# Kernel optimization log

Hardware: AMD Instinct MI355X
Metric: run time of the kernel (lower is better)

## Reference

```python
import jax, jax.numpy as jnp
import numpy as np

N_NODES = 10000
N_EDGES = 160000
HIDDEN = 64
NUM_RBF = 32
Q_DIM = 8
CUTOFF_UPPER = 5.0


def silu(x):
    return x * jax.nn.sigmoid(x)


def tensor_norm(X):
    # X: [n, 3, 3, H] -> [n, H] (Frobenius norm squared over the 3x3 dims)
    return (X * X).sum(axis=(1, 2))


def decompose_tensor(X):
    # X: [n, 3, 3, H] -> I: [n, H] (trace/3), A: antisym [n,3,3,H], S: sym traceless [n,3,3,H]
    eye = jnp.eye(3, dtype=X.dtype)[None, :, :, None]
    I = jnp.einsum('naah->nh', X) / 3.0
    Xt = X.transpose(0, 2, 1, 3)
    A = 0.5 * (X - Xt)
    S = 0.5 * (X + Xt) - I[:, None, None, :] * eye
    return I, A, S


def compose_tensor(I, A, S):
    eye = jnp.eye(3, dtype=A.dtype)[None, :, :, None]
    return I[:, None, None, :] * eye + A + S


def tmm(P, Q):
    # 3x3 matmul per (atom, channel): [n,3,3,H] x [n,3,3,H] -> [n,3,3,H]
    return jnp.einsum('nach,ncbh->nabh', P, Q)


def setup_inputs() -> dict:
    key = jax.random.key(0)
    ks = jax.random.split(key, 16)
    H = HIDDEN
    inp = {
        'X': jax.random.normal(ks[0], (N_NODES, 3, 3, H), jnp.float32),
        'charges': jax.random.normal(ks[1], (N_NODES, Q_DIM), jnp.float32),
        'edge_weight': jax.random.uniform(ks[2], (N_EDGES,), jnp.float32) * CUTOFF_UPPER,
        'edge_attr': jax.random.normal(ks[3], (N_EDGES, NUM_RBF), jnp.float32),
        'edge_index': jax.random.randint(ks[4], (2, N_EDGES), 0, N_NODES, jnp.int32),
    }
    d_in = NUM_RBF + 2 * Q_DIM
    inp['Ws1'] = jax.random.normal(ks[5], (d_in, H), jnp.float32) / np.sqrt(d_in).astype(np.float32)
    inp['bs1'] = jnp.zeros((H,), jnp.float32)
    inp['Ws2'] = jax.random.normal(ks[6], (H, 2 * H), jnp.float32) / np.sqrt(H).astype(np.float32)
    inp['bs2'] = jnp.zeros((2 * H,), jnp.float32)
    inp['Ws3'] = jax.random.normal(ks[7], (2 * H, 3 * H), jnp.float32) / np.sqrt(2 * H).astype(np.float32)
    inp['bs3'] = jnp.zeros((3 * H,), jnp.float32)
    for i in range(6):
        inp['Wt%d' % i] = jax.random.normal(ks[8 + i], (H, H), jnp.float32) / np.sqrt(H).astype(np.float32)
    return inp


def reference(X, charges, edge_weight, edge_attr, Ws1, bs1, Ws2, bs2, Ws3, bs3,
              Wt0, Wt1, Wt2, Wt3, Wt4, Wt5, edge_index):
    H = HIDDEN
    n = X.shape[0]
    row, col = edge_index[0], edge_index[1]
    # cosine cutoff (cutoff_lower = 0)
    C = 0.5 * (jnp.cos(edge_weight * (jnp.pi / CUTOFF_UPPER)) + 1.0)
    C = C * (edge_weight < CUTOFF_UPPER).astype(X.dtype)
    # edge scalar MLP on [rbf, q_i, q_j]
    h = jnp.concatenate([edge_attr, charges[row], charges[col]], axis=-1)
    h = silu(h @ Ws1 + bs1)
    h = silu(h @ Ws2 + bs2)
    h = silu(h @ Ws3 + bs3)
    w = (h * C[:, None]).reshape(h.shape[0], 3, H)  # [E, 3, H]
    # normalize node tensors
    X = X / (tensor_norm(X) + 1.0)[:, None, None, :]
    I, A, S = decompose_tensor(X)
    I = I @ Wt0
    A = A @ Wt1
    S = S @ Wt2
    Y = compose_tensor(I, A, S)
    # message passing: gather I/A/S at source (edge_index[1]), weight per component, scatter-add at dest (edge_index[0])
    eye = jnp.eye(3, dtype=X.dtype)[None, :, :, None]
    msg_e = ((w[:, 0] * I[col])[:, None, None, :] * eye
             + w[:, 1][:, None, None, :] * A[col]
             + w[:, 2][:, None, None, :] * S[col])  # [E, 3, 3, H]
    msg = jax.ops.segment_sum(msg_e, row, num_segments=n)  # [n, 3, 3, H]
    # O(3): C = msg @ Y + Y @ msg (3x3 matmul per channel)
    Cm = tmm(msg, Y) + tmm(Y, msg)
    I2, A2, S2 = decompose_tensor(Cm)
    normp1 = tensor_norm(Cm) + 1.0
    I2 = I2 / normp1
    A2 = A2 / normp1[:, None, None, :]
    S2 = S2 / normp1[:, None, None, :]
    I2 = I2 @ Wt3
    A2 = A2 @ Wt4
    S2 = S2 @ Wt5
    dX = compose_tensor(I2, A2, S2)
    return X + dX + tmm(dX, dX)
```

## Files before the change

kernel.cpp:

```cpp
#include <hip/hip_runtime.h>
#include <math.h>

#define HD 64

typedef _Float16 half8 __attribute__((ext_vector_type(8)));
typedef _Float16 half4v __attribute__((ext_vector_type(4)));
typedef float floatx4 __attribute__((ext_vector_type(4)));

__device__ __forceinline__ float silu_f(float x) {
    return x * __builtin_amdgcn_rcpf(1.0f + __expf(-x));
}

__global__ __launch_bounds__(256) void pre_wconv(
    const float* __restrict__ X,
    const float* __restrict__ Wt0, const float* __restrict__ Wt1, const float* __restrict__ Wt2,
    float* __restrict__ Tn, _Float16* __restrict__ TnH, int N, int nbPre,
    const float* __restrict__ Ws1, const float* __restrict__ Ws2, const float* __restrict__ Ws3,
    _Float16* __restrict__ W1f, _Float16* __restrict__ W2f, _Float16* __restrict__ W3f)
{
    if (blockIdx.x >= nbPre) {
        int id = (blockIdx.x - nbPre) * 256 + threadIdx.x;
        if (id < 4096) {
            int i = id & 7, l = (id >> 3) & 63, t = id >> 9;
            int s = t >> 2, nt = t & 3;
            int k = s * 32 + (l >> 4) * 8 + i;
            int n = nt * 16 + (l & 15);
            W1f[id] = (k < 48) ? (_Float16)Ws1[k * 64 + n] : (_Float16)0.f;
        } else if (id < 4096 + 8192) {
            int j = id - 4096;
            int i = j & 7, l = (j >> 3) & 63, t = j >> 9;
            int s = t >> 3, nt = t & 7;
            int k = s * 32 + (l >> 4) * 8 + i;
            int n = nt * 16 + (l & 15);
            W2f[j] = (_Float16)Ws2[k * 128 + n];
        } else if (id < 4096 + 8192 + 24576) {
            int j = id - 4096 - 8192;
            int i = j & 7, l = (j >> 3) & 63, t = j >> 9;
            int s = t / 12, nt = t % 12;
            int k = s * 32 + (l >> 4) * 8 + i;
            int n = nt * 16 + (l & 15);
            W3f[j] = (_Float16)Ws3[k * 192 + n];
        }
        return;
    }

    int sub = threadIdx.x >> 6;
    int h = threadIdx.x & 63;
    int n = blockIdx.x * 4 + sub;
    int nn = (n < N) ? n : (N - 1);

    const float* Xb = X + (size_t)nn * 9 * HD + h;
    float x[9];
    float nrm = 0.f;
#pragma unroll
    for (int i = 0; i < 9; ++i) { x[i] = Xb[i * HD]; nrm += x[i] * x[i]; }
    float inv = 1.0f / (nrm + 1.0f);
#pragma unroll
    for (int i = 0; i < 9; ++i) x[i] *= inv;

    float I0 = (x[0] + x[4] + x[8]) * (1.0f / 3.0f);
    __shared__ float comp[4][10][HD];
    comp[sub][0][h] = I0;
    comp[sub][1][h] = 0.5f * (x[1] - x[3]);
    comp[sub][2][h] = 0.5f * (x[2] - x[6]);
    comp[sub][3][h] = 0.5f * (x[5] - x[7]);
    comp[sub][4][h] = x[0] - I0;
    comp[sub][5][h] = 0.5f * (x[1] + x[3]);
    comp[sub][6][h] = 0.5f * (x[2] + x[6]);
    comp[sub][7][h] = x[4] - I0;
    comp[sub][8][h] = 0.5f * (x[5] + x[7]);
    comp[sub][9][h] = x[8] - I0;
    __syncthreads();
    float acc[10];
#pragma unroll
    for (int i = 0; i < 10; ++i) acc[i] = 0.f;
    for (int k = 0; k < HD; ++k) {
        float w0 = Wt0[k * HD + h];
        float w1 = Wt1[k * HD + h];
        float w2 = Wt2[k * HD + h];
        acc[0] += comp[sub][0][k] * w0;
        acc[1] += comp[sub][1][k] * w1;
        acc[2] += comp[sub][2][k] * w1;
        acc[3] += comp[sub][3][k] * w1;
#pragma unroll
        for (int j = 0; j < 6; ++j) acc[4 + j] += comp[sub][4 + j][k] * w2;
    }
    if (n < N) {
        float* tp = Tn + (size_t)n * 640 + h;
        _Float16* th = TnH + (size_t)n * 640 + h;
#pragma unroll
        for (int i = 0; i < 10; ++i) {
            tp[i * 64] = acc[i];
            th[i * 64] = (_Float16)acc[i];
        }
    }
}

__global__ __launch_bounds__(256) void count_kernel(
    const int* __restrict__ edge_index, int* __restrict__ cnt, int E)
{
    int e = blockIdx.x * 256 + threadIdx.x;
    if (e < E) atomicAdd(&cnt[edge_index[e]], 1);
}

__global__ __launch_bounds__(1024) void scanA(
    const int* __restrict__ cnt, int* __restrict__ offs, int* __restrict__ partial, int N)
{
    __shared__ int wsum[16];
    int tid = threadIdx.x, wid = tid >> 6, lane = tid & 63;
    int i = blockIdx.x * 1024 + tid;
    int v = (i < N) ? cnt[i] : 0;
    int s = v;
#pragma unroll
    for (int d = 1; d < 64; d <<= 1) {
        int t = __shfl_up(s, d, 64);
        if (lane >= d) s += t;
    }
    if (lane == 63) wsum[wid] = s;
    __syncthreads();
    if (tid == 0) {
        int run = 0;
#pragma unroll
        for (int w = 0; w < 16; ++w) { int t = wsum[w]; wsum[w] = run; run += t; }
        partial[blockIdx.x] = run;
    }
    __syncthreads();
    if (i < N) offs[i] = wsum[wid] + s - v;
}

__global__ __launch_bounds__(256) void scanC(
    int* __restrict__ offs, const int* __restrict__ partial, int* __restrict__ curs,
    int N, int E)
{
    int i = blockIdx.x * 256 + threadIdx.x;
    if (i < N) {
        int b = i >> 10;
        int basev = 0;
        for (int w = 0; w < b; ++w) basev += partial[w];
        int o = offs[i] + basev;
        offs[i] = o;
        curs[i] = o;
    }
    if (i == 0) offs[N] = E;
}

__global__ __launch_bounds__(256) void place_kernel(
    const int* __restrict__ edge_index, int* __restrict__ curs,
    int* __restrict__ rank, int* __restrict__ colP, int E)
{
    int e = blockIdx.x * 256 + threadIdx.x;
    if (e < E) {
        int p = atomicAdd(&curs[edge_index[e]], 1);
        rank[e] = p;
        colP[p] = edge_index[E + e];
    }
}

__global__ __launch_bounds__(256, 5) void mlp_mfma(
    const float* __restrict__ edge_attr, const float* __restrict__ charges,
    const float* __restrict__ edge_weight, const int* __restrict__ edge_index,
    const int* __restrict__ rank,
    const _Float16* __restrict__ W1f, const float* __restrict__ bs1,
    const _Float16* __restrict__ W2f, const float* __restrict__ bs2,
    const _Float16* __restrict__ W3f, const float* __restrict__ bs3,
    _Float16* __restrict__ bufH, int E)
{
    __shared__ __align__(16) _Float16 act[64][200];
    __shared__ float cvsS[64];
    __shared__ int rankSS[64];

    int tid = threadIdx.x;
    int wv = tid >> 6, l = tid & 63;
    int base = blockIdx.x * 64;
    int row16 = l & 15, quad = l >> 4;

#pragma unroll
    for (int i = 0; i < 4; ++i) {
        int slot = tid + i * 256;
        int e_l = slot >> 4, f = slot & 15;
        int e = base + e_l;
        int ee = (e < E) ? e : (E - 1);
        float4 v = make_float4(0.f, 0.f, 0.f, 0.f);
        if (f < 8) {
            v = *(const float4*)(edge_attr + (size_t)ee * 32 + f * 4);
        } else if (f < 10) {
            int r = edge_index[ee];
            v = *(const float4*)(charges + (size_t)r * 8 + (f - 8) * 4);
        } else if (f < 12) {
            int c = edge_index[E + ee];
            v = *(const float4*)(charges + (size_t)c * 8 + (f - 10) * 4);
        }
        half4v hv = { (_Float16)v.x, (_Float16)v.y, (_Float16)v.z, (_Float16)v.w };
        *(half4v*)&act[e_l][f * 4] = hv;
    }
    if (tid < 64) {
        int e = base + tid;
        int ee = (e < E) ? e : (E - 1);
        rankSS[tid] = rank[ee];
        float wgt = edge_weight[ee];
        float cv = 0.5f * (__cosf(wgt * 0.6283185307179586f) + 1.0f);
        cvsS[tid] = (wgt < 5.0f) ? cv : 0.0f;
    }
    __syncthreads();

    {
        half8 w0 = *(const half8*)(W1f + ((size_t)(0 * 4 + wv) * 64 + l) * 8);
        half8 w1 = *(const half8*)(W1f + ((size_t)(1 * 4 + wv) * 64 + l) * 8);
        floatx4 acc1[4];
#pragma unroll
        for (int m = 0; m < 4; ++m) {
            floatx4 c = {0.f, 0.f, 0.f, 0.f};
            c = __builtin_amdgcn_mfma_f32_16x16x32_f16(
                    *(const half8*)&act[m * 16 + row16][quad * 8], w0, c, 0, 0, 0);
            c = __builtin_amdgcn_mfma_f32_16x16x32_f16(
                    *(const half8*)&act[m * 16 + row16][32 + quad * 8], w1, c, 0, 0, 0);
            acc1[m] = c;
        }
        __syncthreads();
        float b = bs1[wv * 16 + row16];
#pragma unroll
        for (int m = 0; m < 4; ++m)
#pragma unroll
            for (int r = 0; r < 4; ++r)
                act[m * 16 + quad * 4 + r][128 + wv * 16 + row16] =
                    (_Float16)silu_f(acc1[m][r] + b);
    }
    __syncthreads();

    {
        floatx4 acc2[4][2];
#pragma unroll
        for (int m = 0; m < 4; ++m)
#pragma unroll
            for (int j = 0; j < 2; ++j) acc2[m][j] = (floatx4){0.f, 0.f, 0.f, 0.f};
#pragma unroll
        for (int s = 0; s < 2; ++s) {
            half8 w0 = *(const half8*)(W2f + ((size_t)(s * 8 + wv * 2 + 0) * 64 + l) * 8);
            half8 w1 = *(const half8*)(W2f + ((size_t)(s * 8 + wv * 2 + 1) * 64 + l) * 8);
#pragma unroll
            for (int m = 0; m < 4; ++m) {
                half8 a = *(const half8*)&act[m * 16 + row16][128 + s * 32 + quad * 8];
                acc2[m][0] = __builtin_amdgcn_mfma_f32_16x16x32_f16(a, w0, acc2[m][0], 0, 0, 0);
                acc2[m][1] = __builtin_amdgcn_mfma_f32_16x16x32_f16(a, w1, acc2[m][1], 0, 0, 0);
            }
        }
        float b0 = bs2[(wv * 2 + 0) * 16 + row16];
        float b1 = bs2[(wv * 2 + 1) * 16 + row16];
#pragma unroll
        for (int m = 0; m < 4; ++m)
#pragma unroll
            for (int r = 0; r < 4; ++r) {
                act[m * 16 + quad * 4 + r][(wv * 2 + 0) * 16 + row16] =
                    (_Float16)silu_f(acc2[m][0][r] + b0);
                act[m * 16 + quad * 4 + r][(wv * 2 + 1) * 16 + row16] =
                    (_Float16)silu_f(acc2[m][1][r] + b1);
            }
    }
    __syncthreads();

    floatx4 acc3[4][3];
#pragma unroll
    for (int m = 0; m < 4; ++m)
#pragma unroll
        for (int j = 0; j < 3; ++j) acc3[m][j] = (floatx4){0.f, 0.f, 0.f, 0.f};
#pragma unroll
    for (int s = 0; s < 4; ++s) {
        half8 w0 = *(const half8*)(W3f + ((size_t)(s * 12 + wv * 3 + 0) * 64 + l) * 8);
        half8 w1 = *(const half8*)(W3f + ((size_t)(s * 12 + wv * 3 + 1) * 64 + l) * 8);
        half8 w2 = *(const half8*)(W3f + ((size_t)(s * 12 + wv * 3 + 2) * 64 + l) * 8);
#pragma unroll
        for (int m = 0; m < 4; ++m) {
            half8 a = *(const half8*)&act[m * 16 + row16][s * 32 + quad * 8];
            acc3[m][0] = __builtin_amdgcn_mfma_f32_16x16x32_f16(a, w0, acc3[m][0], 0, 0, 0);
            acc3[m][1] = __builtin_amdgcn_mfma_f32_16x16x32_f16(a, w1, acc3[m][1], 0, 0, 0);
            acc3[m][2] = __builtin_amdgcn_mfma_f32_16x16x32_f16(a, w2, acc3[m][2], 0, 0, 0);
        }
    }
    __syncthreads();

    {
        float b0 = bs3[(wv * 3 + 0) * 16 + row16];
        float b1 = bs3[(wv * 3 + 1) * 16 + row16];
        float b2 = bs3[(wv * 3 + 2) * 16 + row16];
#pragma unroll
        for (int m = 0; m < 4; ++m) {
#pragma unroll
            for (int r = 0; r < 4; ++r) {
                float cv = cvsS[m * 16 + quad * 4 + r];
                act[m * 16 + quad * 4 + r][(wv * 3 + 0) * 16 + row16] =
                    (_Float16)(silu_f(acc3[m][0][r] + b0) * cv);
                act[m * 16 + quad * 4 + r][(wv * 3 + 1) * 16 + row16] =
                    (_Float16)(silu_f(acc3[m][1][r] + b1) * cv);
                act[m * 16 + quad * 4 + r][(wv * 3 + 2) * 16 + row16] =
                    (_Float16)(silu_f(acc3[m][2][r] + b2) * cv);
            }
        }
    }
    __syncthreads();

    {
        int fr = tid >> 2;
        int ef = base + fr;
        if (ef < E) {
            _Float16* dst = bufH + (size_t)rankSS[fr] * 192;
#pragma unroll
            for (int i = 0; i < 6; ++i) {
                int j = (tid & 3) + i * 4;
                *(half8*)(dst + j * 8) = *(const half8*)&act[fr][j * 8];
            }
        }
    }
}

__global__ __launch_bounds__(256) void msg_kernel(
    const _Float16* __restrict__ bufH, const int* __restrict__ colP,
    const int* __restrict__ offs, const _Float16* __restrict__ TnH,
    float* __restrict__ Mn, int N)
{
    __shared__ float part[4][10][64];
    int qtr = threadIdx.x >> 6;
    int lane = threadIdx.x & 63;
    int n = blockIdx.x;
    int beg = offs[n], end = offs[n + 1];
    int len = end - beg;
    int s0 = beg + (len * qtr) / 4;
    int s1 = beg + (len * (qtr + 1)) / 4;

    float a0 = 0.f, a1 = 0.f, a2 = 0.f, a3 = 0.f, a4 = 0.f;
    float a5 = 0.f, a6 = 0.f, a7 = 0.f, a8 = 0.f, a9 = 0.f;
#pragma unroll 2
    for (int idx = s0; idx < s1; ++idx) {
        int c = colP[idx];
        const _Float16* wp = bufH + (size_t)idx * 192;
        float w0 = (float)wp[lane];
        float w1 = (float)wp[64 + lane];
        float w2 = (float)wp[128 + lane];
        const _Float16* tp = TnH + (size_t)c * 640;
        a0 += w0 * (float)tp[lane];
        a1 += w1 * (float)tp[64 + lane];
        a2 += w1 * (float)tp[128 + lane];
        a3 += w1 * (float)tp[192 + lane];
        a4 += w2 * (float)tp[256 + lane];
        a5 += w2 * (float)tp[320 + lane];
        a6 += w2 * (float)tp[384 + lane];
        a7 += w2 * (float)tp[448 + lane];
        a8 += w2 * (float)tp[512 + lane];
        a9 += w2 * (float)tp[576 + lane];
    }
    part[qtr][0][lane] = a0; part[qtr][1][lane] = a1;
    part[qtr][2][lane] = a2; part[qtr][3][lane] = a3;
    part[qtr][4][lane] = a4; part[qtr][5][lane] = a5;
    part[qtr][6][lane] = a6; part[qtr][7][lane] = a7;
    part[qtr][8][lane] = a8; part[qtr][9][lane] = a9;
    __syncthreads();

    if (qtr < 2) {
        float* mp = Mn + (size_t)n * 640;
#pragma unroll
        for (int j = 0; j < 5; ++j) {
            int c = qtr * 5 + j;
            mp[c * 64 + lane] = (part[0][c][lane] + part[1][c][lane])
                              + (part[2][c][lane] + part[3][c][lane]);
        }
    }
}

__global__ __launch_bounds__(256) void node_post(
    const float* __restrict__ X,
    const float* __restrict__ Tn, const float* __restrict__ Mn,
    const float* __restrict__ Wt3, const float* __restrict__ Wt4, const float* __restrict__ Wt5,
    float* __restrict__ out, int N)
{
    int sub = threadIdx.x >> 6;
    int h = threadIdx.x & 63;
    int n = blockIdx.x * 4 + sub;
    int nn = (n < N) ? n : (N - 1);

    const float* Xb = X + (size_t)nn * 9 * HD + h;
    float x[9];
    float nr = 0.f;
#pragma unroll
    for (int i = 0; i < 9; ++i) { x[i] = Xb[i * HD]; nr += x[i] * x[i]; }
    float xinv = 1.0f / (nr + 1.0f);
#pragma unroll
    for (int i = 0; i < 9; ++i) x[i] *= xinv;

    const float* tp = Tn + (size_t)nn * 640 + h;
    const float* mp = Mn + (size_t)nn * 640 + h;
    float yI = tp[0], mI = mp[0];
    float yA[3], yS[6], mA[3], mS[6];
#pragma unroll
    for (int j = 0; j < 3; ++j) { yA[j] = tp[(1 + j) * 64]; mA[j] = mp[(1 + j) * 64]; }
#pragma unroll
    for (int j = 0; j < 6; ++j) { yS[j] = tp[(4 + j) * 64]; mS[j] = mp[(4 + j) * 64]; }

    float M[3][3] = {
        { mI + mS[0],     mA[0] + mS[1],   mA[1] + mS[2] },
        { -mA[0] + mS[1], mI + mS[3],      mA[2] + mS[4] },
        { -mA[1] + mS[2], -mA[2] + mS[4],  mI + mS[5] } };
    float Y[3][3] = {
        { yI + yS[0],     yA[0] + yS[1],   yA[1] + yS[2] },
        { -yA[0] + yS[1], yI + yS[3],      yA[2] + yS[4] },
        { -yA[1] + yS[2], -yA[2] + yS[4],  yI + yS[5] } };

    float Cm[3][3];
    float nrm = 0.f;
#pragma unroll
    for (int a = 0; a < 3; ++a) {
#pragma unroll
        for (int b = 0; b < 3; ++b) {
            float s = 0.f;
#pragma unroll
            for (int c = 0; c < 3; ++c) s += M[a][c] * Y[c][b] + Y[a][c] * M[c][b];
            Cm[a][b] = s;
            nrm += s * s;
        }
    }
    float inv = 1.0f / (nrm + 1.0f);
    float tr3 = (Cm[0][0] + Cm[1][1] + Cm[2][2]) * (1.0f / 3.0f);

    __shared__ float comp[4][10][HD];
    comp[sub][0][h] = tr3 * inv;
    comp[sub][1][h] = 0.5f * (Cm[0][1] - Cm[1][0]) * inv;
    comp[sub][2][h] = 0.5f * (Cm[0][2] - Cm[2][0]) * inv;
    comp[sub][3][h] = 0.5f * (Cm[1][2] - Cm[2][1]) * inv;
    comp[sub][4][h] = (Cm[0][0] - tr3) * inv;
    comp[sub][5][h] = 0.5f * (Cm[0][1] + Cm[1][0]) * inv;
    comp[sub][6][h] = 0.5f * (Cm[0][2] + Cm[2][0]) * inv;
    comp[sub][7][h] = (Cm[1][1] - tr3) * inv;
    comp[sub][8][h] = 0.5f * (Cm[1][2] + Cm[2][1]) * inv;
    comp[sub][9][h] = (Cm[2][2] - tr3) * inv;
    __syncthreads();

    float acc[10];
#pragma unroll
    for (int i = 0; i < 10; ++i) acc[i] = 0.f;
    for (int k = 0; k < HD; ++k) {
        float w3 = Wt3[k * HD + h];
        float w4 = Wt4[k * HD + h];
        float w5 = Wt5[k * HD + h];
        acc[0] += comp[sub][0][k] * w3;
        acc[1] += comp[sub][1][k] * w4;
        acc[2] += comp[sub][2][k] * w4;
        acc[3] += comp[sub][3][k] * w4;
#pragma unroll
        for (int j = 0; j < 6; ++j) acc[4 + j] += comp[sub][4 + j][k] * w5;
    }
    float D[3][3] = {
        { acc[0] + acc[4],  acc[1] + acc[5],  acc[2] + acc[6] },
        { -acc[1] + acc[5], acc[0] + acc[7],  acc[3] + acc[8] },
        { -acc[2] + acc[6], -acc[3] + acc[8], acc[0] + acc[9] } };

    if (n < N) {
        float* ob = out + (size_t)n * 9 * HD + h;
#pragma unroll
        for (int a = 0; a < 3; ++a) {
#pragma unroll
            for (int b = 0; b < 3; ++b) {
                float s = 0.f;
#pragma unroll
                for (int c = 0; c < 3; ++c) s += D[a][c] * D[c][b];
                ob[(a * 3 + b) * HD] = x[a * 3 + b] + D[a][b] + s;
            }
        }
    }
}

extern "C" void kernel_launch(void* const* d_in, const int* in_sizes, int n_in,
                              void* d_out, int out_size, void* d_ws, size_t ws_size,
                              hipStream_t stream)
{
    const float* X           = (const float*)d_in[0];
    const float* charges     = (const float*)d_in[1];
    const float* edge_weight = (const float*)d_in[2];
    const float* edge_attr   = (const float*)d_in[3];
    const int*   edge_index  = (const int*)d_in[4];
    const float* Ws1 = (const float*)d_in[5];
    const float* bs1 = (const float*)d_in[6];
    const float* Ws2 = (const float*)d_in[7];
    const float* bs2 = (const float*)d_in[8];
    const float* Ws3 = (const float*)d_in[9];
    const float* bs3 = (const float*)d_in[10];
    const float* Wt0 = (const float*)d_in[11];
    const float* Wt1 = (const float*)d_in[12];
    const float* Wt2 = (const float*)d_in[13];
    const float* Wt3 = (const float*)d_in[14];
    const float* Wt4 = (const float*)d_in[15];
    const float* Wt5 = (const float*)d_in[16];

    int N = in_sizes[0] / (9 * HD);
    int E = in_sizes[2];

    float* ws = (float*)d_ws;
    float* Tn  = ws;
    float* Mn  = Tn + (size_t)N * 640;
    _Float16* TnH  = (_Float16*)(Mn + (size_t)N * 640);
    _Float16* bufH = TnH + (size_t)N * 640;
    int* cnt   = (int*)(bufH + (size_t)E * 192);
    int* offs  = cnt + N;
    int* curs  = offs + N + 1;
    int* rank  = curs + N;
    int* colP  = rank + E;
    int* partial = colP + E;
    size_t fofs = ((size_t)((char*)(partial + 64) - (char*)d_ws) + 15) & ~(size_t)15;
    _Float16* W1f = (_Float16*)((char*)d_ws + fofs);
    _Float16* W2f = W1f + 4096;
    _Float16* W3f = W2f + 8192;

    hipMemsetAsync(cnt, 0, (size_t)N * sizeof(int), stream);

    int nbE256 = (E + 255) / 256;
    int nbN1024 = (N + 1023) / 1024;
    count_kernel<<<nbE256, 256, 0, stream>>>(edge_index, cnt, E);
    scanA<<<nbN1024, 1024, 0, stream>>>(cnt, offs, partial, N);
    scanC<<<(N + 255) / 256, 256, 0, stream>>>(offs, partial, curs, N, E);
    place_kernel<<<nbE256, 256, 0, stream>>>(edge_index, curs, rank, colP, E);

    int nbPre = (N + 3) / 4;
    pre_wconv<<<nbPre + 144, 256, 0, stream>>>(X, Wt0, Wt1, Wt2, Tn, TnH, N, nbPre,
                                               Ws1, Ws2, Ws3, W1f, W2f, W3f);

    int nbE64 = (E + 63) / 64;
    mlp_mfma<<<nbE64, 256, 0, stream>>>(edge_attr, charges, edge_weight, edge_index,
                                        rank, W1f, bs1, W2f, bs2, W3f, bs3, bufH, E);

    msg_kernel<<<N, 256, 0, stream>>>(bufH, colP, offs, TnH, Mn, N);

    node_post<<<(N + 3) / 4, 256, 0, stream>>>(X, Tn, Mn, Wt3, Wt4, Wt5, (float*)d_out, N);
}
```

Before: 166.7 us.

## Fuse message aggregation with node post-processing into one kernel

Merges msg_kernel and node_post into a single per-node kernel, so the aggregated message tensor no longer goes to global memory (the Mn buffer is removed) and one launch is saved. All four wavefronts redundantly compute the O(3) product, then split the 10 output-channel matvecs against Wt3/Wt4/Wt5 across wavefronts through shared memory, and split the 9 output components across wavefronts. The redundant per-wave math and the extra syncs add work, and the post stage now runs with one node per 256-thread block.

Result: slower. 186.1 us (+11.7%).

```diff
diff --git a/kernel.cpp b/kernel.cpp
--- a/kernel.cpp
+++ b/kernel.cpp
@@ -312,12 +312,17 @@
     }
 }
 
-__global__ __launch_bounds__(256) void msg_kernel(
+__global__ __launch_bounds__(256) void msg_post(
     const _Float16* __restrict__ bufH, const int* __restrict__ colP,
     const int* __restrict__ offs, const _Float16* __restrict__ TnH,
-    float* __restrict__ Mn, int N)
+    const float* __restrict__ Tn, const float* __restrict__ X,
+    const float* __restrict__ Wt3, const float* __restrict__ Wt4, const float* __restrict__ Wt5,
+    float* __restrict__ out, int N)
 {
     __shared__ float part[4][10][64];
+    __shared__ float compS[10][64];
+    __shared__ float accS[10][64];
+
     int qtr = threadIdx.x >> 6;
     int lane = threadIdx.x & 63;
     int n = blockIdx.x;
@@ -354,114 +359,119 @@
     part[qtr][8][lane] = a8; part[qtr][9][lane] = a9;
     __syncthreads();
 
-    if (qtr < 2) {
-        float* mp = Mn + (size_t)n * 640;
-#pragma unroll
-        for (int j = 0; j < 5; ++j) {
-            int c = qtr * 5 + j;
-            mp[c * 64 + lane] = (part[0][c][lane] + part[1][c][lane])
-                              + (part[2][c][lane] + part[3][c][lane]);
-        }
-    }
-}
-
-__global__ __launch_bounds__(256) void node_post(
-    const float* __restrict__ X,
-    const float* __restrict__ Tn, const float* __restrict__ Mn,
-    const float* __restrict__ Wt3, const float* __restrict__ Wt4, const float* __restrict__ Wt5,
-    float* __restrict__ out, int N)
-{
-    int sub = threadIdx.x >> 6;
-    int h = threadIdx.x & 63;
-    int n = blockIdx.x * 4 + sub;
-    int nn = (n < N) ? n : (N - 1);
-
-    const float* Xb = X + (size_t)nn * 9 * HD + h;
-    float x[9];
-    float nr = 0.f;
-#pragma unroll
-    for (int i = 0; i < 9; ++i) { x[i] = Xb[i * HD]; nr += x[i] * x[i]; }
-    float xinv = 1.0f / (nr + 1.0f);
-#pragma unroll
-    for (int i = 0; i < 9; ++i) x[i] *= xinv;
-
-    const float* tp = Tn + (size_t)nn * 640 + h;
-    const float* mp = Mn + (size_t)nn * 640 + h;
-    float yI = tp[0], mI = mp[0];
-    float yA[3], yS[6], mA[3], mS[6];
-#pragma unroll
-    for (int j = 0; j < 3; ++j) { yA[j] = tp[(1 + j) * 64]; mA[j] = mp[(1 + j) * 64]; }
-#pragma unroll
-    for (int j = 0; j < 6; ++j) { yS[j] = tp[(4 + j) * 64]; mS[j] = mp[(4 + j) * 64]; }
+    float m[10], y[10];
+#pragma unroll
+    for (int i = 0; i < 10; ++i)
+        m[i] = (part[0][i][lane] + part[1][i][lane])
+             + (part[2][i][lane] + part[3][i][lane]);
+    const float* tp = Tn + (size_t)n * 640 + lane;
+#pragma unroll
+    for (int i = 0; i < 10; ++i) y[i] = tp[i * 64];
 
     float M[3][3] = {
-        { mI + mS[0],     mA[0] + mS[1],   mA[1] + mS[2] },
-        { -mA[0] + mS[1], mI + mS[3],      mA[2] + mS[4] },
-        { -mA[1] + mS[2], -mA[2] + mS[4],  mI + mS[5] } };
+        { m[0] + m[4],  m[1] + m[5],  m[2] + m[6] },
+        { -m[1] + m[5], m[0] + m[7],  m[3] + m[8] },
+        { -m[2] + m[6], -m[3] + m[8], m[0] + m[9] } };
     float Y[3][3] = {
-        { yI + yS[0],     yA[0] + yS[1],   yA[1] + yS[2] },
-        { -yA[0] + yS[1], yI + yS[3],      yA[2] + yS[4] },
-        { -yA[1] + yS[2], -yA[2] + yS[4],  yI + yS[5] } };
+        { y[0] + y[4],  y[1] + y[5],  y[2] + y[6] },
+        { -y[1] + y[5], y[0] + y[7],  y[3] + y[8] },
+        { -y[2] + y[6], -y[3] + y[8], y[0] + y[9] } };
 
     float Cm[3][3];
-    float nrm = 0.f;
-#pragma unroll
-    for (int a = 0; a < 3; ++a) {
+    float nrm2 = 0.f;
+#pragma unroll
+    for (int a = 0; a < 3; ++a)
 #pragma unroll
         for (int b = 0; b < 3; ++b) {
             float s = 0.f;
 #pragma unroll
             for (int c = 0; c < 3; ++c) s += M[a][c] * Y[c][b] + Y[a][c] * M[c][b];
             Cm[a][b] = s;
-            nrm += s * s;
-        }
-    }
-    float inv = 1.0f / (nrm + 1.0f);
+            nrm2 += s * s;
+        }
+    float inv = 1.0f / (nrm2 + 1.0f);
     float tr3 = (Cm[0][0] + Cm[1][1] + Cm[2][2]) * (1.0f / 3.0f);
 
-    __shared__ float comp[4][10][HD];
-    comp[sub][0][h] = tr3 * inv;
-    comp[sub][1][h] = 0.5f * (Cm[0][1] - Cm[1][0]) * inv;
-    comp[sub][2][h] = 0.5f * (Cm[0][2] - Cm[2][0]) * inv;
-    comp[sub][3][h] = 0.5f * (Cm[1][2] - Cm[2][1]) * inv;
-    comp[sub][4][h] = (Cm[0][0] - tr3) * inv;
-    comp[sub][5][h] = 0.5f * (Cm[0][1] + Cm[1][0]) * inv;
-    comp[sub][6][h] = 0.5f * (Cm[0][2] + Cm[2][0]) * inv;
-    comp[sub][7][h] = (Cm[1][1] - tr3) * inv;
-    comp[sub][8][h] = 0.5f * (Cm[1][2] + Cm[2][1]) * inv;
-    comp[sub][9][h] = (Cm[2][2] - tr3) * inv;
+    float compv[10];
+    compv[0] = tr3 * inv;
+    compv[1] = 0.5f * (Cm[0][1] - Cm[1][0]) * inv;
+    compv[2] = 0.5f * (Cm[0][2] - Cm[2][0]) * inv;
+    compv[3] = 0.5f * (Cm[1][2] - Cm[2][1]) * inv;
+    compv[4] = (Cm[0][0] - tr3) * inv;
+    compv[5] = 0.5f * (Cm[0][1] + Cm[1][0]) * inv;
+    compv[6] = 0.5f * (Cm[0][2] + Cm[2][0]) * inv;
+    compv[7] = (Cm[1][1] - tr3) * inv;
+    compv[8] = 0.5f * (Cm[1][2] + Cm[2][1]) * inv;
+    compv[9] = (Cm[2][2] - tr3) * inv;
+
+    if (qtr == 0) {
+        compS[0][lane] = compv[0]; compS[1][lane] = compv[1]; compS[2][lane] = compv[2];
+        float A0 = 0.f, A1 = 0.f, A2 = 0.f;
+        for (int k = 0; k < 64; ++k) {
+            float w3 = Wt3[k * 64 + lane];
+            float w4 = Wt4[k * 64 + lane];
+            A0 += compS[0][k] * w3;
+            A1 += compS[1][k] * w4;
+            A2 += compS[2][k] * w4;
+        }
+        accS[0][lane] = A0; accS[1][lane] = A1; accS[2][lane] = A2;
+    } else if (qtr == 1) {
+        compS[3][lane] = compv[3]; compS[4][lane] = compv[4]; compS[5][lane] = compv[5];
+        float A0 = 0.f, A1 = 0.f, A2 = 0.f;
+        for (int k = 0; k < 64; ++k) {
+            float w4 = Wt4[k * 64 + lane];
+            float w5 = Wt5[k * 64 + lane];
+            A0 += compS[3][k] * w4;
+            A1 += compS[4][k] * w5;
+            A2 += compS[5][k] * w5;
+        }
+        accS[3][lane] = A0; accS[4][lane] = A1; accS[5][lane] = A2;
+    } else if (qtr == 2) {
+        compS[6][lane] = compv[6]; compS[7][lane] = compv[7];
+        float A0 = 0.f, A1 = 0.f;
+        for (int k = 0; k < 64; ++k) {
+            float w5 = Wt5[k * 64 + lane];
+            A0 += compS[6][k] * w5;
+            A1 += compS[7][k] * w5;
+        }
+        accS[6][lane] = A0; accS[7][lane] = A1;
+    } else {
+        compS[8][lane] = compv[8]; compS[9][lane] = compv[9];
+        float A0 = 0.f, A1 = 0.f;
+        for (int k = 0; k < 64; ++k) {
+            float w5 = Wt5[k * 64 + lane];
+            A0 += compS[8][k] * w5;
+            A1 += compS[9][k] * w5;
+        }
+        accS[8][lane] = A0; accS[9][lane] = A1;
+    }
     __syncthreads();
 
     float acc[10];
 #pragma unroll
-    for (int i = 0; i < 10; ++i) acc[i] = 0.f;
-    for (int k = 0; k < HD; ++k) {
-        float w3 = Wt3[k * HD + h];
-        float w4 = Wt4[k * HD + h];
-        float w5 = Wt5[k * HD + h];
-        acc[0] += comp[sub][0][k] * w3;
-        acc[1] += comp[sub][1][k] * w4;
-        acc[2] += comp[sub][2][k] * w4;
-        acc[3] += comp[sub][3][k] * w4;
-#pragma unroll
-        for (int j = 0; j < 6; ++j) acc[4 + j] += comp[sub][4 + j][k] * w5;
-    }
+    for (int i = 0; i < 10; ++i) acc[i] = accS[i][lane];
     float D[3][3] = {
         { acc[0] + acc[4],  acc[1] + acc[5],  acc[2] + acc[6] },
         { -acc[1] + acc[5], acc[0] + acc[7],  acc[3] + acc[8] },
         { -acc[2] + acc[6], -acc[3] + acc[8], acc[0] + acc[9] } };
 
-    if (n < N) {
-        float* ob = out + (size_t)n * 9 * HD + h;
-#pragma unroll
-        for (int a = 0; a < 3; ++a) {
-#pragma unroll
-            for (int b = 0; b < 3; ++b) {
-                float s = 0.f;
-#pragma unroll
-                for (int c = 0; c < 3; ++c) s += D[a][c] * D[c][b];
-                ob[(a * 3 + b) * HD] = x[a * 3 + b] + D[a][b] + s;
-            }
+    const float* Xb = X + (size_t)n * 576 + lane;
+    float xr[9];
+    float nr = 0.f;
+#pragma unroll
+    for (int i = 0; i < 9; ++i) { xr[i] = Xb[i * 64]; nr += xr[i] * xr[i]; }
+    float xinv = 1.0f / (nr + 1.0f);
+
+    float* ob = out + (size_t)n * 576 + lane;
+#pragma unroll
+    for (int j0 = 0; j0 < 9; j0 += 4) {
+        int j = j0 + qtr;
+        if (j < 9) {
+            int a = j / 3, b = j % 3;
+            float s = 0.f;
+#pragma unroll
+            for (int c = 0; c < 3; ++c) s += D[a][c] * D[c][b];
+            ob[j * 64] = xr[j] * xinv + D[a][b] + s;
         }
     }
 }
@@ -493,8 +503,7 @@
 
     float* ws = (float*)d_ws;
     float* Tn  = ws;
-    float* Mn  = Tn + (size_t)N * 640;
-    _Float16* TnH  = (_Float16*)(Mn + (size_t)N * 640);
+    _Float16* TnH  = (_Float16*)(Tn + (size_t)N * 640);
     _Float16* bufH = TnH + (size_t)N * 640;
     int* cnt   = (int*)(bufH + (size_t)E * 192);
     int* offs  = cnt + N;
@@ -524,7 +533,6 @@
     mlp_mfma<<<nbE64, 256, 0, stream>>>(edge_attr, charges, edge_weight, edge_index,
                                         rank, W1f, bs1, W2f, bs2, W3f, bs3, bufH, E);
 
-    msg_kernel<<<N, 256, 0, stream>>>(bufH, colP, offs, TnH, Mn, N);
-
-    node_post<<<(N + 3) / 4, 256, 0, stream>>>(X, Tn, Mn, Wt3, Wt4, Wt5, (float*)d_out, N);
-}
+    msg_post<<<N, 256, 0, stream>>>(bufH, colP, offs, TnH, Tn, X,
+                                    Wt3, Wt4, Wt5, (float*)d_out, N);
+}
```

## Fuse CSR build into node-prep and MLP kernels, single-block scan

Applied to the files above, without the earlier changes.

Edge-count atomics are folded into the node preprocessing launch as extra blocks, the two-pass scan becomes one single-block looping scan, and edge placement (the atomicAdd on the cursor plus the colP write) moves into the MLP kernel prologue. This cuts the CSR build from four launches down to one small scan launch and drops the rank buffer. A __syncthreads in the MLP first layer is also removed. The risk is that the single-block scan serialises work over N, and removing that barrier may let the layer-1 output writes overlap reads of the input columns (they write to a different region, columns 128+, so it is likely safe).

Result: faster. 159.3 us (-4.4%).

```diff
diff --git a/kernel.cpp b/kernel.cpp
--- a/kernel.cpp
+++ b/kernel.cpp
@@ -11,13 +11,19 @@
     return x * __builtin_amdgcn_rcpf(1.0f + __expf(-x));
 }
 
-__global__ __launch_bounds__(256) void pre_wconv(
+__global__ __launch_bounds__(256) void pre_wconv_count(
     const float* __restrict__ X,
     const float* __restrict__ Wt0, const float* __restrict__ Wt1, const float* __restrict__ Wt2,
     float* __restrict__ Tn, _Float16* __restrict__ TnH, int N, int nbPre,
     const float* __restrict__ Ws1, const float* __restrict__ Ws2, const float* __restrict__ Ws3,
-    _Float16* __restrict__ W1f, _Float16* __restrict__ W2f, _Float16* __restrict__ W3f)
+    _Float16* __restrict__ W1f, _Float16* __restrict__ W2f, _Float16* __restrict__ W3f,
+    const int* __restrict__ edge_index, int* __restrict__ cnt, int E)
 {
+    if (blockIdx.x >= nbPre + 144) {
+        int e = (blockIdx.x - nbPre - 144) * 256 + threadIdx.x;
+        if (e < E) atomicAdd(&cnt[edge_index[e]], 1);
+        return;
+    }
     if (blockIdx.x >= nbPre) {
         int id = (blockIdx.x - nbPre) * 256 + threadIdx.x;
         if (id < 4096) {
@@ -96,70 +102,43 @@
     }
 }
 
-__global__ __launch_bounds__(256) void count_kernel(
-    const int* __restrict__ edge_index, int* __restrict__ cnt, int E)
+__global__ __launch_bounds__(1024) void scan_kernel(
+    const int* __restrict__ cnt, int* __restrict__ offs, int* __restrict__ curs, int N)
 {
-    int e = blockIdx.x * 256 + threadIdx.x;
-    if (e < E) atomicAdd(&cnt[edge_index[e]], 1);
-}
-
-__global__ __launch_bounds__(1024) void scanA(
-    const int* __restrict__ cnt, int* __restrict__ offs, int* __restrict__ partial, int N)
-{
-    __shared__ int wsum[16];
+    __shared__ int partials[16];
+    __shared__ int base_s;
     int tid = threadIdx.x, wid = tid >> 6, lane = tid & 63;
-    int i = blockIdx.x * 1024 + tid;
-    int v = (i < N) ? cnt[i] : 0;
-    int s = v;
-#pragma unroll
-    for (int d = 1; d < 64; d <<= 1) {
-        int t = __shfl_up(s, d, 64);
-        if (lane >= d) s += t;
-    }
-    if (lane == 63) wsum[wid] = s;
-    __syncthreads();
-    if (tid == 0) {
-        int run = 0;
-#pragma unroll
-        for (int w = 0; w < 16; ++w) { int t = wsum[w]; wsum[w] = run; run += t; }
-        partial[blockIdx.x] = run;
-    }
-    __syncthreads();
-    if (i < N) offs[i] = wsum[wid] + s - v;
-}
-
-__global__ __launch_bounds__(256) void scanC(
-    int* __restrict__ offs, const int* __restrict__ partial, int* __restrict__ curs,
-    int N, int E)
-{
-    int i = blockIdx.x * 256 + threadIdx.x;
-    if (i < N) {
-        int b = i >> 10;
-        int basev = 0;
-        for (int w = 0; w < b; ++w) basev += partial[w];
-        int o = offs[i] + basev;
-        offs[i] = o;
-        curs[i] = o;
-    }
-    if (i == 0) offs[N] = E;
-}
-
-__global__ __launch_bounds__(256) void place_kernel(
-    const int* __restrict__ edge_index, int* __restrict__ curs,
-    int* __restrict__ rank, int* __restrict__ colP, int E)
-{
-    int e = blockIdx.x * 256 + threadIdx.x;
-    if (e < E) {
-        int p = atomicAdd(&curs[edge_index[e]], 1);
-        rank[e] = p;
-        colP[p] = edge_index[E + e];
-    }
+    if (tid == 0) base_s = 0;
+    __syncthreads();
+    for (int start = 0; start < N; start += 1024) {
+        int i = start + tid;
+        int v = (i < N) ? cnt[i] : 0;
+        int s = v;
+#pragma unroll
+        for (int d = 1; d < 64; d <<= 1) {
+            int t = __shfl_up(s, d, 64);
+            if (lane >= d) s += t;
+        }
+        if (lane == 63) partials[wid] = s;
+        __syncthreads();
+        if (tid == 0) {
+            int run = base_s;
+#pragma unroll
+            for (int w = 0; w < 16; ++w) { int t = partials[w]; partials[w] = run; run += t; }
+            base_s = run;
+        }
+        __syncthreads();
+        int excl = partials[wid] + s - v;
+        if (i < N) { offs[i] = excl; curs[i] = excl; }
+        __syncthreads();
+    }
+    if (tid == 0) offs[N] = base_s;
 }
 
 __global__ __launch_bounds__(256, 5) void mlp_mfma(
     const float* __restrict__ edge_attr, const float* __restrict__ charges,
     const float* __restrict__ edge_weight, const int* __restrict__ edge_index,
-    const int* __restrict__ rank,
+    int* __restrict__ curs, int* __restrict__ colP,
     const _Float16* __restrict__ W1f, const float* __restrict__ bs1,
     const _Float16* __restrict__ W2f, const float* __restrict__ bs2,
     const _Float16* __restrict__ W3f, const float* __restrict__ bs3,
@@ -195,8 +174,16 @@
     }
     if (tid < 64) {
         int e = base + tid;
-        int ee = (e < E) ? e : (E - 1);
-        rankSS[tid] = rank[ee];
+        bool valid = (e < E);
+        int ee = valid ? e : (E - 1);
+        int row = edge_index[ee];
+        int col = edge_index[E + ee];
+        int rk = 0;
+        if (valid) {
+            rk = atomicAdd(&curs[row], 1);
+            colP[rk] = col;
+        }
+        rankSS[tid] = rk;
         float wgt = edge_weight[ee];
         float cv = 0.5f * (__cosf(wgt * 0.6283185307179586f) + 1.0f);
         cvsS[tid] = (wgt < 5.0f) ? cv : 0.0f;
@@ -216,7 +203,6 @@
                     *(const half8*)&act[m * 16 + row16][32 + quad * 8], w1, c, 0, 0, 0);
             acc1[m] = c;
         }
-        __syncthreads();
         float b = bs1[wv * 16 + row16];
 #pragma unroll
         for (int m = 0; m < 4; ++m)
@@ -499,30 +485,25 @@
     int* cnt   = (int*)(bufH + (size_t)E * 192);
     int* offs  = cnt + N;
     int* curs  = offs + N + 1;
-    int* rank  = curs + N;
-    int* colP  = rank + E;
-    int* partial = colP + E;
-    size_t fofs = ((size_t)((char*)(partial + 64) - (char*)d_ws) + 15) & ~(size_t)15;
+    int* colP  = curs + N;
+    size_t fofs = ((size_t)((char*)(colP + E) - (char*)d_ws) + 15) & ~(size_t)15;
     _Float16* W1f = (_Float16*)((char*)d_ws + fofs);
     _Float16* W2f = W1f + 4096;
     _Float16* W3f = W2f + 8192;
 
     hipMemsetAsync(cnt, 0, (size_t)N * sizeof(int), stream);
 
+    int nbPre = (N + 3) / 4;
     int nbE256 = (E + 255) / 256;
-    int nbN1024 = (N + 1023) / 1024;
-    count_kernel<<<nbE256, 256, 0, stream>>>(edge_index, cnt, E);
-    scanA<<<nbN1024, 1024, 0, stream>>>(cnt, offs, partial, N);
-    scanC<<<(N + 255) / 256, 256, 0, stream>>>(offs, partial, curs, N, E);
-    place_kernel<<<nbE256, 256, 0, stream>>>(edge_index, curs, rank, colP, E);
-
-    int nbPre = (N + 3) / 4;
-    pre_wconv<<<nbPre + 144, 256, 0, stream>>>(X, Wt0, Wt1, Wt2, Tn, TnH, N, nbPre,
-                                               Ws1, Ws2, Ws3, W1f, W2f, W3f);
+    pre_wconv_count<<<nbPre + 144 + nbE256, 256, 0, stream>>>(
+        X, Wt0, Wt1, Wt2, Tn, TnH, N, nbPre,
+        Ws1, Ws2, Ws3, W1f, W2f, W3f, edge_index, cnt, E);
+
+    scan_kernel<<<1, 1024, 0, stream>>>(cnt, offs, curs, N);
 
     int nbE64 = (E + 63) / 64;
     mlp_mfma<<<nbE64, 256, 0, stream>>>(edge_attr, charges, edge_weight, edge_index,
-                                        rank, W1f, bs1, W2f, bs2, W3f, bs3, bufH, E);
+                                        curs, colP, W1f, bs1, W2f, bs2, W3f, bs3, bufH, E);
 
     msg_kernel<<<N, 256, 0, stream>>>(bufH, colP, offs, TnH, Mn, N);
 
```
